# Kernel tuning notes

Measured on AMD Instinct MI355X. Metric: run time of the kernel, lower is better.

Reference implementation:

```python
import jax, jax.numpy as jnp
import numpy as np

N = 50000      # nodes
E = 800000     # edges (avg degree 16)
F_IN = 256     # input feature dim
H, D = 4, 32   # heads, per-head dim
HD = H * D
K = 25000      # SAGPool keeps ceil(0.5*N) nodes
C = 2          # classes
SLOPE = 0.4
NEG = -1e9

def _gat(x, src, dst, valid, n, W, b, al, ar):
    # DGL GATConv: fc -> per-head attn logits -> edge softmax over dst -> weighted sum
    h = (x @ W).reshape(-1, H, D)                      # [n,H,D]
    el = jnp.einsum('nhd,hd->nh', h, al)
    er = jnp.einsum('nhd,hd->nh', h, ar)
    e = jax.nn.leaky_relu(el[src] + er[dst], SLOPE)    # [E,H]
    e = jnp.where(valid[:, None], e, NEG)
    m = jnp.maximum(jax.ops.segment_max(e, dst, num_segments=n), NEG)
    ex = jnp.exp(e - m[dst]) * valid[:, None].astype(x.dtype)
    s = jax.ops.segment_sum(ex, dst, num_segments=n)
    alpha = ex / jnp.maximum(s[dst], 1e-16)            # [E,H] edge softmax
    out = jax.ops.segment_sum(alpha[:, :, None] * h[src], dst, num_segments=n)
    return out + b.reshape(1, H, D), alpha

def _sagpool(x, src, dst, valid, n, k, Wc, bc):
    # score = GraphConv(in,1) with symmetric norm; keep top-k nodes, scale by tanh(score)
    vf = valid.astype(x.dtype)
    deg_o = jnp.maximum(jax.ops.segment_sum(vf, src, num_segments=n), 1.0)
    deg_i = jnp.maximum(jax.ops.segment_sum(vf, dst, num_segments=n), 1.0)
    h = (x @ Wc) * (deg_o ** -0.5)[:, None]
    agg = jax.ops.segment_sum(h[src] * vf[:, None], dst, num_segments=n)
    score = (agg * (deg_i ** -0.5)[:, None] + bc)[:, 0]   # [n]
    vals, perm = jax.lax.top_k(score, k)
    xk = x[perm] * jnp.tanh(vals)[:, None]                # [k,F]
    new_id = jnp.full((n,), -1, jnp.int32).at[perm].set(jnp.arange(k, dtype=jnp.int32))
    ns, nd = new_id[src], new_id[dst]
    nv = valid & (ns >= 0) & (nd >= 0)                    # edges fully inside subgraph
    return xk, jnp.where(nv, ns, 0), jnp.where(nv, nd, 0), nv

def setup_inputs():
    key = jax.random.key(0)
    k = jax.random.split(key, 18)
    rn = lambda i, shape, scale: jax.random.normal(k[i], shape, jnp.float32) * scale
    return {
        "feature": rn(0, (N, F_IN), 1.0),
        "strength": jax.random.uniform(k[1], (E,), dtype=jnp.float32),
        "W0": rn(2, (F_IN, HD), F_IN ** -0.5), "b0": jnp.zeros((HD,), jnp.float32),
        "al0": rn(3, (H, D), 0.1), "ar0": rn(4, (H, D), 0.1),
        "Wc0": rn(5, (HD, 1), HD ** -0.5), "bc0": jnp.zeros((1,), jnp.float32),
        "W1": rn(6, (HD, HD), HD ** -0.5), "b1": jnp.zeros((HD,), jnp.float32),
        "al1": rn(7, (H, D), 0.1), "ar1": rn(8, (H, D), 0.1),
        "gate_W": rn(9, (D, 1), D ** -0.5), "gate_b": jnp.zeros((1,), jnp.float32),
        "cls_W": rn(10, (D, C), D ** -0.5), "cls_b": jnp.zeros((C,), jnp.float32),
        "src": jax.random.randint(k[11], (E,), 0, N, dtype=jnp.int32),
        "dst": jax.random.randint(k[12], (E,), 0, N, dtype=jnp.int32),
    }

def reference(feature, strength, W0, b0, al0, ar0, Wc0, bc0, W1, b1, al1, ar1,
              gate_W, gate_b, cls_W, cls_b, src, dst):
    valid0 = jnp.ones((E,), bool)
    h0, _ = _gat(feature, src, dst, valid0, N, W0, b0, al0, ar0)
    x = h0.reshape(N, HD)                                  # flatten(1)
    x1, s1, d1, v1 = _sagpool(x, src, dst, valid0, N, K, Wc0, bc0)
    h1, atten = _gat(x1, s1, d1, v1, K, W1, b1, al1, ar1)  # get_attention=True
    strength1 = strength * v1.astype(strength.dtype)       # edata carried into subgraph (masked)
    res = h1.mean(axis=1)                                  # [K,D] mean over heads
    gate = jax.nn.softmax(res @ gate_W + gate_b, axis=0)   # [K,1] GlobalAttentionPooling
    readout = jnp.sum(gate * res, axis=0, keepdims=True)   # [1,D]
    lbl_pred = readout @ cls_W + cls_b                     # [1,C]
    return (readout, lbl_pred, atten, strength1)
```

## Files before the change

### kernel.cpp

```cpp
#include <hip/hip_runtime.h>
#include <stdint.h>

#define NN 50000
#define EE 800000
#define FIN 256
#define HD 128
#define DD 32
#define KK 25000
#define SLOPEF 0.4f
#define NEGF (-1e9f)
#define ATT_OFF 34
#define STR_OFF (34 + EE * 4)
#define CW 128

#define BCH 32
#define EPC (EE / BCH)

__device__ __forceinline__ unsigned fkey(float x) {
    unsigned u = __float_as_uint(x);
    return (u & 0x80000000u) ? ~u : (u | 0x80000000u);
}
__device__ __forceinline__ float unfkey(unsigned k) {
    unsigned u = (k & 0x80000000u) ? (k ^ 0x80000000u) : ~k;
    return __uint_as_float(u);
}
__device__ __forceinline__ float lrelu(float v) { return v > 0.f ? v : SLOPEF * v; }

__device__ __forceinline__ void ast(int* pp, int v) {
    __hip_atomic_store(pp, v, __ATOMIC_RELAXED, __HIP_MEMORY_SCOPE_AGENT);
}
__device__ __forceinline__ int ald(const int* pp) {
    return __hip_atomic_load(pp, __ATOMIC_RELAXED, __HIP_MEMORY_SCOPE_AGENT);
}
__device__ __forceinline__ void astu(unsigned* pp, unsigned v) {
    __hip_atomic_store(pp, v, __ATOMIC_RELAXED, __HIP_MEMORY_SCOPE_AGENT);
}
__device__ __forceinline__ unsigned aldu(const unsigned* pp) {
    return __hip_atomic_load(pp, __ATOMIC_RELAXED, __HIP_MEMORY_SCOPE_AGENT);
}

__device__ __forceinline__ void gridbar(int* cnt, int* flag, int nb) {
    __syncthreads();
    __threadfence();
    if (threadIdx.x == 0) {
        int old = __hip_atomic_fetch_add(cnt, 1, __ATOMIC_ACQ_REL, __HIP_MEMORY_SCOPE_AGENT);
        if (old == nb - 1) {
            __hip_atomic_store(flag, 1, __ATOMIC_RELEASE, __HIP_MEMORY_SCOPE_AGENT);
        } else {
            while (__hip_atomic_load(flag, __ATOMIC_ACQUIRE, __HIP_MEMORY_SCOPE_AGENT) == 0) {
                __builtin_amdgcn_s_sleep(8);
            }
        }
    }
    __syncthreads();
}

__device__ __forceinline__ int blockscan(int v, int* lds) {
    int lane = threadIdx.x & 63, w = threadIdx.x >> 6;
    int incl = v;
#pragma unroll
    for (int o = 1; o < 64; o <<= 1) { int u = __shfl_up(incl, o); if (lane >= o) incl += u; }
    __syncthreads();
    if (lane == 63) lds[w] = incl;
    __syncthreads();
    int add = 0;
    for (int i = 0; i < w; i++) add += lds[i];
    return incl + add;
}

struct P {
    const float *feature, *strength, *W0, *b0, *al0, *ar0, *Wc0, *bc0;
    const float *W1, *b1, *al1, *ar1, *gW, *gb, *cW, *cb;
    const int *src, *dst;
    double *Zacc, *racc;
    int *cnt;
    unsigned *gmaxk;
    unsigned *rs;
    int *bar;
    unsigned *binsHi, *binsLo;
    unsigned *keys;
    unsigned char *degc_i, *degc_o;
    unsigned *cb0;
    int *dsum;
    int *csr_src, *rank, *off0, *sel, *slot, *list, *bsum;
    float *z0, *el0, *er0, *q4, *m0f, *s0f, *b0wc, *hc, *score, *xk, *z1;
    float *el1, *er1, *m1f, *s1f, *res, *g, *tscale;
    float *out;
};

#define BM 128
#define BN 64
#define BK 16
__device__ void gemm_body(
    const float* __restrict__ A, const float* __restrict__ B, float* __restrict__ C,
    int M, int Kd,
    const float* __restrict__ al, const float* __restrict__ ar,
    float* __restrict__ el, float* __restrict__ er,
    const float* __restrict__ Wc, float* __restrict__ q4,
    int bx, int by) {
    __shared__ float As[BK][BM + 4];
    __shared__ float Bs[BK][BN];
    int bm = by * BM, bn = bx * BN;
    int tid = threadIdx.x;
    int tr = tid >> 4, tc = tid & 15;
    int lrow = tid >> 1;
    int arow = (bm + lrow < M) ? (bm + lrow) : -1;
    float acc[8][4] = {};
    for (int k0 = 0; k0 < Kd; k0 += BK) {
        {
            int col = (tid & 1) << 3;
            float4 v0 = {0.f,0.f,0.f,0.f}, v1 = {0.f,0.f,0.f,0.f};
            if (arow >= 0) {
                const float* ap = A + (size_t)arow * Kd + k0 + col;
                v0 = *(const float4*)ap; v1 = *(const float4*)(ap + 4);
            }
            As[col + 0][lrow] = v0.x; As[col + 1][lrow] = v0.y;
            As[col + 2][lrow] = v0.z; As[col + 3][lrow] = v0.w;
            As[col + 4][lrow] = v1.x; As[col + 5][lrow] = v1.y;
            As[col + 6][lrow] = v1.z; As[col + 7][lrow] = v1.w;
        }
        {
            int kr = tid >> 4, col = (tid & 15) << 2;
            float4 v = *(const float4*)(B + (size_t)(k0 + kr) * HD + bn + col);
            *(float4*)&Bs[kr][col] = v;
        }
        __syncthreads();
#pragma unroll
        for (int kk = 0; kk < BK; kk++) {
            float a[8], b[4];
#pragma unroll
            for (int i = 0; i < 8; i++) a[i] = As[kk][tr * 8 + i];
#pragma unroll
            for (int j = 0; j < 4; j++) b[j] = Bs[kk][tc * 4 + j];
#pragma unroll
            for (int i = 0; i < 8; i++)
#pragma unroll
                for (int j = 0; j < 4; j++) acc[i][j] = fmaf(a[i], b[j], acc[i][j]);
        }
        __syncthreads();
    }
#pragma unroll
    for (int i = 0; i < 8; i++) {
        int gr = bm + tr * 8 + i;
        if (gr < M) {
            float4 v = {acc[i][0], acc[i][1], acc[i][2], acc[i][3]};
            *(float4*)(C + (size_t)gr * HD + bn + tc * 4) = v;
        }
    }
    int head = bx * 2 + (tc >> 3);
    int dbase = (tc & 7) * 4;
    const float* alh = al + head * 32 + dbase;
    const float* arh = ar + head * 32 + dbase;
    float a0 = alh[0], a1 = alh[1], a2 = alh[2], a3 = alh[3];
    float r0 = arh[0], r1 = arh[1], r2 = arh[2], r3 = arh[3];
    float w0 = 0.f, w1 = 0.f, w2 = 0.f, w3 = 0.f;
    if (Wc) {
        const float* wch = Wc + head * 32 + dbase;
        w0 = wch[0]; w1 = wch[1]; w2 = wch[2]; w3 = wch[3];
    }
#pragma unroll
    for (int i = 0; i < 8; i++) {
        int gr = bm + tr * 8 + i;
        float pe = acc[i][0]*a0 + acc[i][1]*a1 + acc[i][2]*a2 + acc[i][3]*a3;
        float pr = acc[i][0]*r0 + acc[i][1]*r1 + acc[i][2]*r2 + acc[i][3]*r3;
        float pq = acc[i][0]*w0 + acc[i][1]*w1 + acc[i][2]*w2 + acc[i][3]*w3;
#pragma unroll
        for (int o = 1; o < 8; o <<= 1) {
            pe += __shfl_xor(pe, o); pr += __shfl_xor(pr, o); pq += __shfl_xor(pq, o);
        }
        if ((tc & 7) == 0 && gr < M) {
            el[gr * 4 + head] = pe; er[gr * 4 + head] = pr;
            if (Wc) q4[gr * 4 + head] = pq;
        }
    }
}

__global__ __launch_bounds__(256) void k_count0(P p) {
    __shared__ unsigned hist[NN / 4];
    int blk = blockIdx.x;
    int isD = blk < BCH;
    int c = isD ? blk : blk - BCH;
    for (int w = threadIdx.x; w < NN / 4; w += 256) hist[w] = 0u;
    __syncthreads();
    int j0 = c * EPC, j1 = j0 + EPC;
    if (isD) {
        for (int e = j0 + (int)threadIdx.x; e < j1; e += 256) {
            int d = p.dst[e];
            unsigned sh = (unsigned)(d & 3) * 8u;
            unsigned old = atomicAdd(&hist[d >> 2], 1u << sh);
            p.rank[e] = (int)((old >> sh) & 0xffu);
        }
    } else {
        for (int e = j0 + (int)threadIdx.x; e < j1; e += 256) {
            int s = p.src[e];
            atomicAdd(&hist[s >> 2], 1u << ((unsigned)(s & 3) * 8u));
        }
    }
    __syncthreads();
    unsigned* o32 = (unsigned*)((isD ? p.degc_i : p.degc_o) + (size_t)c * NN);
    for (int w = threadIdx.x; w < NN / 4; w += 256) o32[w] = hist[w];
}

#define SB 64
__global__ __launch_bounds__(1024) void k_scan0(P p) {
    __shared__ int lds[16];
    __shared__ int ldsg[SB];
    __shared__ int ldsb[2];
    int tid = threadIdx.x, blk = blockIdx.x;
    int i = blk * 1024 + tid;
    int tot = 0;
    if (i < NN) {
#pragma unroll
        for (int c = 0; c < BCH; c++) tot += p.degc_i[(size_t)c * NN + i];
    }
    int incl = blockscan(tot, lds);
    if (tid == 1023) ast(&p.bsum[blk], incl);
    gridbar(&p.bar[14], &p.bar[15], SB);
    if (tid < SB) ldsg[tid] = ald(&p.bsum[tid]);
    __syncthreads();
    if (tid == 0) {
        int pre = 0, all = 0;
        for (int b2 = 0; b2 < SB; b2++) { if (b2 < blk) pre += ldsg[b2]; all += ldsg[b2]; }
        ldsb[0] = pre; ldsb[1] = all;
    }
    __syncthreads();
    if (i < NN) {
        int base = ldsb[0] + incl - tot;
        p.off0[i] = base;
        unsigned run = (unsigned)base;
        int s = 0;
#pragma unroll
        for (int c = 0; c < BCH; c++) {
            p.cb0[(size_t)c * NN + i] = run;
            run += p.degc_i[(size_t)c * NN + i];
            s += p.degc_o[(size_t)c * NN + i];
        }
        p.dsum[i] = s;
    }
    if (blk == 0 && tid == 0) p.off0[NN] = ldsb[1];
}

#define G0B 782
#define GB_E 3125
__global__ __launch_bounds__(256) void k_g0sc(P p) {
    int blk = blockIdx.x;
    if (blk < G0B) {
        gemm_body(p.feature, p.W0, p.z0, NN, FIN, p.al0, p.ar0, p.el0, p.er0,
                  p.Wc0, p.q4, blk & 1, blk >> 1);
    } else if (blk < G0B + GB_E) {
        int e = (blk - G0B) * 256 + threadIdx.x;
        if (e < EE) {
            int c = e / EPC;
            int d = p.dst[e];
            unsigned pos = p.cb0[(size_t)c * NN + d] + (unsigned)p.rank[e];
            p.csr_src[pos] = p.src[e];
        }
    } else {
        int l = threadIdx.x;
        if (l < 64) {
            float t = p.b0[l] * p.Wc0[l] + p.b0[l + 64] * p.Wc0[l + 64];
#pragma unroll
            for (int o = 1; o < 64; o <<= 1) t += __shfl_xor(t, o);
            if (l == 0) p.b0wc[0] = t;
        }
    }
}

__global__ __launch_bounds__(256) void k_fgatlite(
    const int* __restrict__ off, const int* __restrict__ csrs,
    const float* __restrict__ el, const float* __restrict__ er,
    const float* __restrict__ q4, const int* __restrict__ dsum,
    const float* __restrict__ b0wc,
    float* __restrict__ hc, float* __restrict__ m0f, float* __restrict__ s0f) {
    int wv = threadIdx.x >> 6, lane = threadIdx.x & 63;
    int v = blockIdx.x * 4 + wv;
    int b = off[v], e = off[v + 1], deg = e - b;
    int h = lane >> 4, sub = lane & 15;
    float erh = er[(size_t)v * 4 + h];
    float m = NEGF;
    for (int li = sub; li < deg; li += 16) {
        int s = csrs[b + li];
        m = fmaxf(m, lrelu(el[(size_t)s * 4 + h] + erh));
    }
#pragma unroll
    for (int o = 1; o < 16; o <<= 1) m = fmaxf(m, __shfl_xor(m, o));
    float ssum = 0.f, hq = 0.f;
    for (int li = sub; li < deg; li += 16) {
        int s = csrs[b + li];
        float ex = expf(lrelu(el[(size_t)s * 4 + h] + erh) - m);
        ssum += ex;
        hq = fmaf(ex, q4[(size_t)s * 4 + h], hq);
    }
#pragma unroll
    for (int o = 1; o < 16; o <<= 1) { ssum += __shfl_xor(ssum, o); hq += __shfl_xor(hq, o); }
    if (sub == 0) { m0f[v * 4 + h] = m; s0f[v * 4 + h] = ssum; }
    float t = hq / fmaxf(ssum, 1e-16f);
    t += __shfl_xor(t, 16);
    t += __shfl_xor(t, 32);
    if (lane == 0)
        hc[v] = (t + b0wc[0]) / sqrtf(fmaxf((float)dsum[v], 1.f));
}

#define PB 64
__global__ __launch_bounds__(1024) void k_pool(P p) {
    __shared__ int lds[16];
    __shared__ int ldsg[PB];
    __shared__ int ldsb[2];
    int tid = threadIdx.x, blk = blockIdx.x;
    int gtid = blk * 1024 + tid;
    if (gtid < NN) {
        int b = p.off0[gtid], en = p.off0[gtid + 1];
        float acc = 0.f;
        for (int i = b; i < en; i++) acc += p.hc[p.csr_src[i]];
        float dg = fmaxf((float)(en - b), 1.f);
        float sc = acc / sqrtf(dg) + p.bc0[0];
        p.score[gtid] = sc;
        unsigned k_ = fkey(sc);
        p.keys[gtid] = k_;
        atomicAdd(&p.binsHi[k_ >> 16], 1u);
    }
    gridbar(&p.bar[0], &p.bar[1], PB);
    {
        int cnt = (int)p.binsHi[gtid];
        int incl = blockscan(cnt, lds);
        if (tid == 1023) ast(&p.bsum[64 + blk], incl);
        gridbar(&p.bar[2], &p.bar[3], PB);
        if (tid < PB) ldsg[tid] = ald(&p.bsum[64 + tid]);
        __syncthreads();
        if (tid == 0) {
            int ab = 0;
            for (int b2 = PB - 1; b2 > blk; b2--) ab += ldsg[b2];
            ldsb[0] = ab; ldsb[1] = ldsg[blk];
        }
        __syncthreads();
        int above = ldsb[0] + (ldsb[1] - incl);
        if (above < KK && above + cnt >= KK) {
            astu(&p.rs[64], (unsigned)gtid);
            astu(&p.rs[65], (unsigned)(KK - above));
        }
    }
    gridbar(&p.bar[4], &p.bar[5], PB);
    unsigned hib = aldu(&p.rs[64]);
    if (gtid < NN) {
        unsigned k_ = p.keys[gtid];
        if ((k_ >> 16) == hib) atomicAdd(&p.binsLo[k_ & 0xFFFFu], 1u);
    }
    gridbar(&p.bar[6], &p.bar[7], PB);
    int K2 = (int)aldu(&p.rs[65]);
    {
        int cnt = (int)p.binsLo[gtid];
        int incl = blockscan(cnt, lds);
        if (tid == 1023) ast(&p.bsum[128 + blk], incl);
        gridbar(&p.bar[8], &p.bar[9], PB);
        if (tid < PB) ldsg[tid] = ald(&p.bsum[128 + tid]);
        __syncthreads();
        if (tid == 0) {
            int ab = 0;
            for (int b2 = PB - 1; b2 > blk; b2--) ab += ldsg[b2];
            ldsb[0] = ab; ldsb[1] = ldsg[blk];
        }
        __syncthreads();
        int above = ldsb[0] + (ldsb[1] - incl);
        if (above < K2 && above + cnt >= K2) {
            astu(&p.rs[0], (hib << 16) | (unsigned)gtid);
            astu(&p.rs[1], (unsigned)(K2 - above));
        }
    }
    gridbar(&p.bar[10], &p.bar[11], PB);
    unsigned pivot = aldu(&p.rs[0]);
    int need = (int)aldu(&p.rs[1]);
    unsigned k_ = (gtid < NN) ? p.keys[gtid] : 0u;
    int tie = (gtid < NN && k_ == pivot) ? 1 : 0;
    int incl = blockscan(tie, lds);
    if (tid == 1023) ast(&p.bsum[192 + blk], incl);
    gridbar(&p.bar[12], &p.bar[13], PB);
    if (tid < PB) ldsg[tid] = ald(&p.bsum[192 + tid]);
    __syncthreads();
    if (tid == 0) {
        int pre = 0;
        for (int b2 = 0; b2 < blk; b2++) pre += ldsg[b2];
        ldsb[0] = pre;
    }
    __syncthreads();
    int rank = ldsb[0] + incl - tie;
    if (gtid < NN) {
        int selv = (k_ > pivot) || (tie && rank < need);
        if (selv) {
            int idx = atomicAdd(p.cnt, 1);
            p.list[idx] = gtid;
            p.slot[gtid] = idx;
            p.tscale[idx] = tanhf(p.score[gtid]);
        } else {
            p.slot[gtid] = -1;
        }
    }
}

__global__ __launch_bounds__(256) void k_fgatx(
    const int* __restrict__ list, const float* __restrict__ tscale,
    const int* __restrict__ off, const int* __restrict__ csrs,
    const float* __restrict__ el, const float* __restrict__ er,
    const float* __restrict__ m0f, const float* __restrict__ s0f,
    const float* __restrict__ z, const float* __restrict__ b0,
    float* __restrict__ xk) {
    __shared__ int ssrc[4][CW];
    __shared__ float sexp[4][CW][4];
    int wv = threadIdx.x >> 6, lane = threadIdx.x & 63;
    int i = blockIdx.x * 4 + wv;
    int v = list[i];
    int b = off[v], e = off[v + 1], deg = e - b;
    int h = lane >> 4, sub = lane & 15;
    float erh = er[(size_t)v * 4 + h];
    float mh = m0f[v * 4 + h];
    for (int li = sub; li < deg; li += 16) {
        int s = csrs[b + li];
        if (h == 0 && li < CW) ssrc[wv][li] = s;
        if (li < CW) sexp[wv][li][h] = expf(lrelu(el[(size_t)s * 4 + h] + erh) - mh);
    }
    __syncthreads();
    int h0 = lane >> 5, h1 = h0 + 2;
    float s0 = s0f[v * 4 + h0], s1 = s0f[v * 4 + h1];
    float m0 = m0f[v * 4 + h0], m1 = m0f[v * 4 + h1];
    float er0v = er[(size_t)v * 4 + h0], er1v = er[(size_t)v * 4 + h1];
    int c0 = lane, c1 = lane + 64;
    float acc0 = 0.f, acc1 = 0.f;
    for (int li = 0; li < deg; li++) {
        int s; float w0, w1;
        if (li < CW) {
            s = ssrc[wv][li];
            w0 = sexp[wv][li][h0]; w1 = sexp[wv][li][h1];
        } else {
            s = csrs[b + li];
            w0 = expf(lrelu(el[(size_t)s * 4 + h0] + er0v) - m0);
            w1 = expf(lrelu(el[(size_t)s * 4 + h1] + er1v) - m1);
        }
        int su = __builtin_amdgcn_readfirstlane(s);
        const float* zr = z + (size_t)su * HD;
        acc0 = fmaf(w0, zr[c0], acc0);
        acc1 = fmaf(w1, zr[c1], acc1);
    }
    float ts = tscale[i];
    float* xr = xk + (size_t)i * HD;
    xr[c0] = (acc0 / fmaxf(s0, 1e-16f) + b0[c0]) * ts;
    xr[c1] = (acc1 / fmaxf(s1, 1e-16f) + b0[c1]) * ts;
}

#define G1B 392
__global__ __launch_bounds__(256) void k_gemm1(P p) {
    gemm_body(p.xk, p.W1, p.z1, KK, HD, p.al1, p.ar1, p.el1, p.er1,
              nullptr, nullptr, blockIdx.x & 1, blockIdx.x >> 1);
}

__global__ __launch_bounds__(256) void k_fgat2(P p) {
    __shared__ int ssrc[4][CW];
    __shared__ float sexp[4][CW][4];
    int wv = threadIdx.x >> 6, lane = threadIdx.x & 63;
    int i = blockIdx.x * 4 + wv;
    int v = p.list[i];
    int b = p.off0[v], e = p.off0[v + 1], deg = e - b;
    int h = lane >> 4, sub = lane & 15;
    float4 er4 = *(const float4*)(p.er1 + (size_t)i * 4);
    float erh = ((const float*)&er4)[h];
    float m = NEGF;
    for (int li = sub; li < deg; li += 16) {
        int so = p.csr_src[b + li];
        int ss = p.slot[so];
        if (h == 0 && li < CW) ssrc[wv][li] = ss;
        if (ss >= 0) m = fmaxf(m, lrelu(p.el1[(size_t)ss * 4 + h] + erh));
    }
#pragma unroll
    for (int o = 1; o < 16; o <<= 1) m = fmaxf(m, __shfl_xor(m, o));
    float ssum = 0.f;
    for (int li = sub; li < deg; li += 16) {
        int so = p.csr_src[b + li];
        int ss = p.slot[so];
        float x = (ss >= 0) ? expf(lrelu(p.el1[(size_t)ss * 4 + h] + erh) - m) : 0.f;
        if (li < CW) sexp[wv][li][h] = x;
        ssum += x;
    }
#pragma unroll
    for (int o = 1; o < 16; o <<= 1) ssum += __shfl_xor(ssum, o);
    if (sub == 0) { p.m1f[i * 4 + h] = m; p.s1f[i * 4 + h] = ssum; }
    __syncthreads();
    int h0 = lane >> 5, h1 = h0 + 2;
    float m0 = __shfl(m, h0 << 4), m1 = __shfl(m, h1 << 4);
    float s0 = __shfl(ssum, h0 << 4), s1 = __shfl(ssum, h1 << 4);
    int c0 = lane, c1 = lane + 64;
    float acc0 = 0.f, acc1 = 0.f;
    for (int li = 0; li < deg; li++) {
        int s; float w0, w1;
        if (li < CW) {
            s = ssrc[wv][li];
            if (s < 0) continue;
            w0 = sexp[wv][li][h0]; w1 = sexp[wv][li][h1];
        } else {
            int so = p.csr_src[b + li];
            s = p.slot[so];
            if (s < 0) continue;
            w0 = expf(lrelu(p.el1[(size_t)s * 4 + h0] + ((const float*)&er4)[h0]) - m0);
            w1 = expf(lrelu(p.el1[(size_t)s * 4 + h1] + ((const float*)&er4)[h1]) - m1);
        }
        int su = __builtin_amdgcn_readfirstlane(s);
        const float* zr = p.z1 + (size_t)su * HD;
        acc0 = fmaf(w0, zr[c0], acc0);
        acc1 = fmaf(w1, zr[c1], acc1);
    }
    float xc0 = acc0 / fmaxf(s0, 1e-16f) + p.b1[c0];
    float xc1 = acc1 / fmaxf(s1, 1e-16f) + p.b1[c1];
    float t = xc0 + xc1;
    t += __shfl_xor(t, 32);
    float pg = 0.f;
    if (lane < 32) {
        float r = 0.25f * t;
        p.res[(size_t)i * 32 + lane] = r;
        pg = r * p.gW[lane];
    }
#pragma unroll
    for (int o = 1; o < 32; o <<= 1) pg += __shfl_xor(pg, o);
    if (lane == 0) p.g[i] = pg + p.gb[0];
}

__global__ void k_ealpha1(P p) {
    int e = blockIdx.x * blockDim.x + threadIdx.x;
    if (e >= EE) return;
    int ds = p.slot[p.src[e]], dd = p.slot[p.dst[e]];
    float a[4] = {0.f, 0.f, 0.f, 0.f};
    float st = 0.f;
    if (ds >= 0 && dd >= 0) {
        float4 es = *(const float4*)(p.el1 + ds * 4);
        float4 ed = *(const float4*)(p.er1 + dd * 4);
        float l[4] = {lrelu(es.x + ed.x), lrelu(es.y + ed.y), lrelu(es.z + ed.z), lrelu(es.w + ed.w)};
#pragma unroll
        for (int h = 0; h < 4; h++) {
            float m = p.m1f[dd * 4 + h];
            float ex = expf(l[h] - m);
            a[h] = ex / fmaxf(p.s1f[dd * 4 + h], 1e-16f);
        }
        st = p.strength[e];
    }
    float* o = p.out + ATT_OFF + (size_t)e * 4;
    *(float2*)(o) = make_float2(a[0], a[1]);
    *(float2*)(o + 2) = make_float2(a[2], a[3]);
    p.out[STR_OFF + e] = st;
}

#define RB 104
__global__ __launch_bounds__(256) void k_read(P p) {
    __shared__ float redf[256];
    __shared__ double vred[256];
    __shared__ double zred[8];
    __shared__ float rb2[32];
    int t = threadIdx.x;
    float m = -3.4e38f;
    for (int i = blockIdx.x * 256 + t; i < KK; i += RB * 256) m = fmaxf(m, p.g[i]);
    redf[t] = m;
    __syncthreads();
    for (int o = 128; o > 0; o >>= 1) { if (t < o) redf[t] = fmaxf(redf[t], redf[t + o]); __syncthreads(); }
    if (t == 0) atomicMax(p.gmaxk, fkey(redf[0]));
    gridbar(&p.bar[16], &p.bar[17], RB);
    int il = t >> 5, d = t & 31;
    float gm = unfkey(aldu(p.gmaxk));
    double accv = 0.0, accw = 0.0;
    for (int i = blockIdx.x * 8 + il; i < KK; i += RB * 8) {
        float w = expf(p.g[i] - gm);
        accv += (double)(w * p.res[(size_t)i * 32 + d]);
        if (d == 0) accw += (double)w;
    }
    vred[t] = accv;
    if (d == 0) zred[il] = accw;
    __syncthreads();
    if (il == 0) {
        double s = 0;
#pragma unroll
        for (int k2 = 0; k2 < 8; k2++) s += vred[k2 * 32 + d];
        atomicAdd(&p.racc[d], s);
    }
    if (t == 32) {
        double z2 = 0;
#pragma unroll
        for (int k2 = 0; k2 < 8; k2++) z2 += zred[k2];
        atomicAdd(p.Zacc, z2);
    }
    gridbar(&p.bar[18], &p.bar[19], RB);
    if (blockIdx.x == 0) {
        double Z = *p.Zacc;
        if (t < 32) {
            float r = (float)(p.racc[t] / Z);
            p.out[t] = r;
            rb2[t] = r;
        }
        __syncthreads();
        if (t < 2) {
            float s = 0.f;
            for (int dd2 = 0; dd2 < 32; dd2++) s += rb2[dd2] * p.cW[dd2 * 2 + t];
            p.out[32 + t] = s + p.cb[t];
        }
    }
}

extern "C" void kernel_launch(void* const* d_in, const int* in_sizes, int n_in,
                              void* d_out, int out_size, void* d_ws, size_t ws_size,
                              hipStream_t stream) {
    (void)in_sizes; (void)n_in; (void)out_size; (void)ws_size;
    P p;
    p.feature  = (const float*)d_in[0];
    p.strength = (const float*)d_in[1];
    p.W0  = (const float*)d_in[2];  p.b0  = (const float*)d_in[3];
    p.al0 = (const float*)d_in[4];  p.ar0 = (const float*)d_in[5];
    p.Wc0 = (const float*)d_in[6];  p.bc0 = (const float*)d_in[7];
    p.W1  = (const float*)d_in[8];  p.b1  = (const float*)d_in[9];
    p.al1 = (const float*)d_in[10]; p.ar1 = (const float*)d_in[11];
    p.gW  = (const float*)d_in[12]; p.gb  = (const float*)d_in[13];
    p.cW  = (const float*)d_in[14]; p.cb  = (const float*)d_in[15];
    p.src = (const int*)d_in[16];   p.dst = (const int*)d_in[17];
    p.out = (float*)d_out;

    char* ws = (char*)d_ws;
    size_t off = 0;
    auto alloc = [&](size_t bytes) -> void* {
        void* r = ws + off;
        off = (off + bytes + 255) & ~(size_t)255;
        return r;
    };
    p.Zacc  = (double*)alloc(8);
    p.racc  = (double*)alloc(32 * 8);
    p.cnt   = (int*)alloc(4);
    p.gmaxk = (unsigned*)alloc(4);
    p.rs    = (unsigned*)alloc(128 * 4);
    p.bar   = (int*)alloc(32 * 4);
    p.binsHi = (unsigned*)alloc(65536 * 4);
    p.binsLo = (unsigned*)alloc(65536 * 4);
    size_t zbytes = off;
    p.degc_i = (unsigned char*)alloc((size_t)BCH * NN);
    p.degc_o = (unsigned char*)alloc((size_t)BCH * NN);
    p.cb0 = (unsigned*)alloc((size_t)BCH * NN * 4);
    p.dsum = (int*)alloc((size_t)NN * 4);
    p.z0 = (float*)alloc((size_t)NN * HD * 4);
    p.xk = (float*)alloc((size_t)KK * HD * 4);
    p.z1 = (float*)alloc((size_t)KK * HD * 4);
    p.csr_src = (int*)alloc((size_t)EE * 4);
    p.rank    = (int*)alloc((size_t)EE * 4);
    p.el0 = (float*)alloc((size_t)NN * 4 * 4);
    p.er0 = (float*)alloc((size_t)NN * 4 * 4);
    p.q4  = (float*)alloc((size_t)NN * 4 * 4);
    p.m0f = (float*)alloc((size_t)NN * 4 * 4);
    p.s0f = (float*)alloc((size_t)NN * 4 * 4);
    p.b0wc = (float*)alloc(4);
    p.off0 = (int*)alloc((size_t)(NN + 1) * 4);
    p.bsum = (int*)alloc(256 * 4);
    p.hc    = (float*)alloc((size_t)NN * 4);
    p.score = (float*)alloc((size_t)NN * 4);
    p.keys  = (unsigned*)alloc((size_t)NN * 4);
    p.sel   = (int*)alloc((size_t)NN * 4);
    p.slot  = (int*)alloc((size_t)NN * 4);
    p.list  = (int*)alloc((size_t)KK * 4);
    p.tscale = (float*)alloc((size_t)KK * 4);
    p.el1 = (float*)alloc((size_t)KK * 4 * 4);
    p.er1 = (float*)alloc((size_t)KK * 4 * 4);
    p.m1f = (float*)alloc((size_t)KK * 4 * 4);
    p.s1f = (float*)alloc((size_t)KK * 4 * 4);
    p.res = (float*)alloc((size_t)KK * DD * 4);
    p.g   = (float*)alloc((size_t)KK * 4);

    hipMemsetAsync(d_ws, 0, zbytes, stream);

    k_count0<<<2 * BCH, 256, 0, stream>>>(p);
    k_scan0<<<SB, 1024, 0, stream>>>(p);
    k_g0sc<<<G0B + GB_E + 1, 256, 0, stream>>>(p);
    k_fgatlite<<<NN / 4, 256, 0, stream>>>(p.off0, p.csr_src, p.el0, p.er0, p.q4,
                                           p.dsum, p.b0wc, p.hc, p.m0f, p.s0f);

    k_pool<<<PB, 1024, 0, stream>>>(p);

    k_fgatx<<<KK / 4, 256, 0, stream>>>(p.list, p.tscale, p.off0, p.csr_src,
                                        p.el0, p.er0, p.m0f, p.s0f, p.z0, p.b0, p.xk);
    k_gemm1<<<G1B, 256, 0, stream>>>(p);
    k_fgat2<<<KK / 4, 256, 0, stream>>>(p);
    k_ealpha1<<<GB_E, 256, 0, stream>>>(p);

    k_read<<<RB, 256, 0, stream>>>(p);
}
```

Measured before the change: 619.6 us.

## Replace two-level 16-bit radix top-k select with 4-pass 8-bit LDS-histogram select

The top-k pivot search in the pooling kernel moves from two 65536-bin global histograms, each followed by a grid-wide scan, to four 8-bit radix passes. Each pass builds a block-local LDS histogram and flushes it to a small 256-bin global array, and every block then scans the 256 bins itself without a second grid barrier. Scores and keys stay in registers, which drops the score and key global buffers and shrinks the zeroed workspace. The cost is four grid barriers plus LDS atomics in place of two histogram rounds, leaving five barriers in total instead of seven.

```diff
diff --git a/kernel.cpp b/kernel.cpp
--- a/kernel.cpp
+++ b/kernel.cpp
@@ -32,9 +32,6 @@
 __device__ __forceinline__ int ald(const int* pp) {
     return __hip_atomic_load(pp, __ATOMIC_RELAXED, __HIP_MEMORY_SCOPE_AGENT);
 }
-__device__ __forceinline__ void astu(unsigned* pp, unsigned v) {
-    __hip_atomic_store(pp, v, __ATOMIC_RELAXED, __HIP_MEMORY_SCOPE_AGENT);
-}
 __device__ __forceinline__ unsigned aldu(const unsigned* pp) {
     return __hip_atomic_load(pp, __ATOMIC_RELAXED, __HIP_MEMORY_SCOPE_AGENT);
 }
@@ -75,15 +72,13 @@
     double *Zacc, *racc;
     int *cnt;
     unsigned *gmaxk;
-    unsigned *rs;
     int *bar;
-    unsigned *binsHi, *binsLo;
-    unsigned *keys;
+    unsigned *bins4;
     unsigned char *degc_i, *degc_o;
     unsigned *cb0;
     int *dsum;
-    int *csr_src, *rank, *off0, *sel, *slot, *list, *bsum;
-    float *z0, *el0, *er0, *q4, *m0f, *s0f, *b0wc, *hc, *score, *xk, *z1;
+    int *csr_src, *rank, *off0, *slot, *list, *bsum;
+    float *z0, *el0, *er0, *q4, *m0f, *s0f, *b0wc, *hc, *xk, *z1;
     float *el1, *er1, *m1f, *s1f, *res, *g, *tscale;
     float *out;
 };
@@ -304,77 +299,57 @@
 #define PB 64
 __global__ __launch_bounds__(1024) void k_pool(P p) {
     __shared__ int lds[16];
+    __shared__ unsigned sb[256];
     __shared__ int ldsg[PB];
     __shared__ int ldsb[2];
+    __shared__ unsigned selres[2];
     int tid = threadIdx.x, blk = blockIdx.x;
     int gtid = blk * 1024 + tid;
-    if (gtid < NN) {
+    int valid = (gtid < NN);
+    float sc = 0.f;
+    unsigned key = 0u;
+    if (valid) {
         int b = p.off0[gtid], en = p.off0[gtid + 1];
         float acc = 0.f;
         for (int i = b; i < en; i++) acc += p.hc[p.csr_src[i]];
         float dg = fmaxf((float)(en - b), 1.f);
-        float sc = acc / sqrtf(dg) + p.bc0[0];
-        p.score[gtid] = sc;
-        unsigned k_ = fkey(sc);
-        p.keys[gtid] = k_;
-        atomicAdd(&p.binsHi[k_ >> 16], 1u);
-    }
-    gridbar(&p.bar[0], &p.bar[1], PB);
-    {
-        int cnt = (int)p.binsHi[gtid];
-        int incl = blockscan(cnt, lds);
-        if (tid == 1023) ast(&p.bsum[64 + blk], incl);
-        gridbar(&p.bar[2], &p.bar[3], PB);
-        if (tid < PB) ldsg[tid] = ald(&p.bsum[64 + tid]);
-        __syncthreads();
-        if (tid == 0) {
-            int ab = 0;
-            for (int b2 = PB - 1; b2 > blk; b2--) ab += ldsg[b2];
-            ldsb[0] = ab; ldsb[1] = ldsg[blk];
-        }
-        __syncthreads();
-        int above = ldsb[0] + (ldsb[1] - incl);
-        if (above < KK && above + cnt >= KK) {
-            astu(&p.rs[64], (unsigned)gtid);
-            astu(&p.rs[65], (unsigned)(KK - above));
-        }
-    }
-    gridbar(&p.bar[4], &p.bar[5], PB);
-    unsigned hib = aldu(&p.rs[64]);
-    if (gtid < NN) {
-        unsigned k_ = p.keys[gtid];
-        if ((k_ >> 16) == hib) atomicAdd(&p.binsLo[k_ & 0xFFFFu], 1u);
-    }
-    gridbar(&p.bar[6], &p.bar[7], PB);
-    int K2 = (int)aldu(&p.rs[65]);
-    {
-        int cnt = (int)p.binsLo[gtid];
-        int incl = blockscan(cnt, lds);
-        if (tid == 1023) ast(&p.bsum[128 + blk], incl);
-        gridbar(&p.bar[8], &p.bar[9], PB);
-        if (tid < PB) ldsg[tid] = ald(&p.bsum[128 + tid]);
-        __syncthreads();
-        if (tid == 0) {
-            int ab = 0;
-            for (int b2 = PB - 1; b2 > blk; b2--) ab += ldsg[b2];
-            ldsb[0] = ab; ldsb[1] = ldsg[blk];
-        }
-        __syncthreads();
-        int above = ldsb[0] + (ldsb[1] - incl);
-        if (above < K2 && above + cnt >= K2) {
-            astu(&p.rs[0], (hib << 16) | (unsigned)gtid);
-            astu(&p.rs[1], (unsigned)(K2 - above));
-        }
-    }
-    gridbar(&p.bar[10], &p.bar[11], PB);
-    unsigned pivot = aldu(&p.rs[0]);
-    int need = (int)aldu(&p.rs[1]);
-    unsigned k_ = (gtid < NN) ? p.keys[gtid] : 0u;
-    int tie = (gtid < NN && k_ == pivot) ? 1 : 0;
-    int incl = blockscan(tie, lds);
-    if (tid == 1023) ast(&p.bsum[192 + blk], incl);
-    gridbar(&p.bar[12], &p.bar[13], PB);
-    if (tid < PB) ldsg[tid] = ald(&p.bsum[192 + tid]);
+        sc = acc / sqrtf(dg) + p.bc0[0];
+        key = fkey(sc);
+    }
+    unsigned pref = 0u;
+    int K = KK;
+#pragma unroll
+    for (int l = 0; l < 4; l++) {
+        int sh = 24 - 8 * l;
+        if (tid < 256) sb[tid] = 0u;
+        __syncthreads();
+        int cand = valid && ((l == 0) || ((key >> (sh + 8)) == pref));
+        if (cand) atomicAdd(&sb[(key >> sh) & 0xFFu], 1u);
+        __syncthreads();
+        if (tid < 256 && sb[tid]) atomicAdd(&p.bins4[l * 256 + tid], sb[tid]);
+        gridbar(&p.bar[2 * l], &p.bar[2 * l + 1], PB);
+        unsigned cnt = (tid < 256) ? aldu(&p.bins4[l * 256 + tid]) : 0u;
+        int incl = blockscan((int)cnt, lds);
+        if (tid == 255) ldsb[0] = incl;
+        __syncthreads();
+        int total = ldsb[0];
+        int above = total - incl;
+        if (tid < 256 && above < K && above + (int)cnt >= K) {
+            selres[0] = (unsigned)tid;
+            selres[1] = (unsigned)(K - above);
+        }
+        __syncthreads();
+        pref = (pref << 8) | selres[0];
+        K = (int)selres[1];
+        __syncthreads();
+    }
+    unsigned pivot = pref;
+    int need = K;
+    int tie = (valid && key == pivot) ? 1 : 0;
+    int incl2 = blockscan(tie, lds);
+    if (tid == 1023) ast(&p.bsum[blk], incl2);
+    gridbar(&p.bar[8], &p.bar[9], PB);
+    if (tid < PB) ldsg[tid] = ald(&p.bsum[tid]);
     __syncthreads();
     if (tid == 0) {
         int pre = 0;
@@ -382,14 +357,14 @@
         ldsb[0] = pre;
     }
     __syncthreads();
-    int rank = ldsb[0] + incl - tie;
-    if (gtid < NN) {
-        int selv = (k_ > pivot) || (tie && rank < need);
+    int rank = ldsb[0] + incl2 - tie;
+    if (valid) {
+        int selv = (key > pivot) || (tie && rank < need);
         if (selv) {
             int idx = atomicAdd(p.cnt, 1);
             p.list[idx] = gtid;
             p.slot[gtid] = idx;
-            p.tscale[idx] = tanhf(p.score[gtid]);
+            p.tscale[idx] = tanhf(sc);
         } else {
             p.slot[gtid] = -1;
         }
@@ -626,10 +601,8 @@
     p.racc  = (double*)alloc(32 * 8);
     p.cnt   = (int*)alloc(4);
     p.gmaxk = (unsigned*)alloc(4);
-    p.rs    = (unsigned*)alloc(128 * 4);
     p.bar   = (int*)alloc(32 * 4);
-    p.binsHi = (unsigned*)alloc(65536 * 4);
-    p.binsLo = (unsigned*)alloc(65536 * 4);
+    p.bins4 = (unsigned*)alloc(4 * 256 * 4);
     size_t zbytes = off;
     p.degc_i = (unsigned char*)alloc((size_t)BCH * NN);
     p.degc_o = (unsigned char*)alloc((size_t)BCH * NN);
@@ -649,9 +622,6 @@
     p.off0 = (int*)alloc((size_t)(NN + 1) * 4);
     p.bsum = (int*)alloc(256 * 4);
     p.hc    = (float*)alloc((size_t)NN * 4);
-    p.score = (float*)alloc((size_t)NN * 4);
-    p.keys  = (unsigned*)alloc((size_t)NN * 4);
-    p.sel   = (int*)alloc((size_t)NN * 4);
     p.slot  = (int*)alloc((size_t)NN * 4);
     p.list  = (int*)alloc((size_t)KK * 4);
     p.tscale = (float*)alloc((size_t)KK * 4);
```

New measurement: 588.8 us. 5.0% less time.
